# Performance work log

Measured on AMD Instinct MI355X. Metric: run time of the kernel, lower is better.

The kernel has to match this reference:

```python
import jax, jax.numpy as jnp
import numpy as np


def setup_inputs() -> dict:
    key = jax.random.key(0)
    k1, k2, k3, k4 = jax.random.split(key, 4)
    B, C, T = 32, 512, 1024
    N, D = 64, 512
    scale = 1.0 / np.sqrt(C)
    x = jax.random.normal(k1, (B, C, T), dtype=jnp.float32)
    subjects = jax.random.randint(k2, (B,), 0, N, dtype=jnp.int64)
    weights = jax.random.normal(k3, (N, C, D), dtype=jnp.float32) * scale
    bias = jax.random.normal(k4, (N, D), dtype=jnp.float32) * scale
    return {"x": x, "subjects": subjects, "weights": weights, "bias": bias}


def reference(x, subjects, weights, bias):
    # gather mode: per-example projection matrix, then batched GEMM
    # x: (B, C, T); weights[subjects]: (B, C, D) -> out: (B, D, T)
    w = weights[subjects]                      # (B, C, D)
    out = jnp.einsum('bct,bcd->bdt', x, w)
    out = out + bias[subjects][:, :, None]     # (B, D, 1) broadcast over T
    return out
```

## Files before the change

kernel.cpp:

```cpp
#include <hip/hip_runtime.h>
#include <hip/hip_bf16.h>

#define B_N 32
#define C_K 512
#define T_N 1024
#define D_M 512

constexpr int BM = 128, BN = 128, BK = 32;
constexpr int SA = 36;
constexpr int KSTEPS = C_K / BK;
constexpr int BUFO = BM * SA;

typedef __attribute__((ext_vector_type(4))) float  floatx4;
typedef __attribute__((ext_vector_type(4))) short  shortx4;
typedef __attribute__((ext_vector_type(8))) short  shortx8;
typedef __attribute__((ext_vector_type(2))) unsigned int uintx2;

__device__ __forceinline__ unsigned pk2(float a, float b) {
  __hip_bfloat162 h = __float22bfloat162_rn(make_float2(a, b));
  union { __hip_bfloat162 v; unsigned u; } c; c.v = h; return c.u;
}

__device__ __forceinline__ void wg_barrier() {
  asm volatile("s_waitcnt lgkmcnt(0)" ::: "memory");
  __builtin_amdgcn_s_barrier();
  __builtin_amdgcn_sched_barrier(0);
}

__global__ __launch_bounds__(512, 4)
void subject_gemm(const float* __restrict__ x, const int* __restrict__ subjects,
                  const float* __restrict__ weights, const float* __restrict__ bias,
                  float* __restrict__ out)
{
  __shared__ __align__(16) short lds_a[2][BUFO];
  __shared__ __align__(16) short lds_b[2][BUFO];

  const int bid  = blockIdx.x;
  const int xcd  = bid & 7;
  const int s    = bid >> 3;
  const int b    = xcd * 4 + (s & 3);
  const int tile = s >> 2;
  const int tm = tile >> 3, tn = tile & 7;
  const int m0 = tm * BM, n0 = tn * BN;
  const int nb = subjects[b];

  const float* __restrict__ Wp = weights + (size_t)nb * C_K * D_M;
  const float* __restrict__ Xp = x + (size_t)b * C_K * T_N;

  const int tid  = threadIdx.x;
  const int lane = tid & 63;
  const int wave = tid >> 6;

  const bool isA = (wave < 4);
  const int  wv  = wave & 3;
  const int  o   = lane >> 5;
  const int  mg  = lane & 31;
  const int  kq  = 2 * wv + o;
  const float* gsrc = isA ? (Wp + (size_t)(4 * kq) * D_M + (m0 + 4 * mg))
                          : (Xp + (size_t)(4 * kq) * T_N + (n0 + 4 * mg));
  const int gs = isA ? D_M : T_N;
  const int swz = (mg >> 2) & 3;
  short* const wbase = (isA ? &lds_a[0][0] : &lds_b[0][0])
                       + (4 * mg) * SA + 4 * (kq ^ swz);

  const int wm = (wave & 1) * 64, wn = (wave >> 1) * 32;
  const int w1 = (wave >> 1) & 1;
  const int l15 = lane & 15, q = lane >> 4;

  floatx4 acc[4][2] = {};
  floatx4 vA[4], vB[4];

  auto loads = [&](floatx4 (&v)[4]) {
    #pragma unroll
    for (int jj = 0; jj < 4; ++jj)
      v[jj] = *(const floatx4*)(gsrc + (size_t)jj * gs);
    gsrc += (size_t)BK * gs;
  };
  auto cvt_store = [&](const floatx4 (&v)[4], int p) {
    short* wdst = wbase + p * BUFO;
    #pragma unroll
    for (int r = 0; r < 4; ++r) {
      uintx2 pk = { pk2(v[0][r], v[1][r]), pk2(v[2][r], v[3][r]) };
      *(uintx2*)(wdst + r * SA) = pk;
    }
  };
  auto compute = [&](int p) {
    const short* pa = &lds_a[p][0] + (wm + l15) * SA;
    const short* pb = &lds_b[p][0] + (wn + l15) * SA;
    shortx8 af[4], bg[2];
    #pragma unroll
    for (int i = 0; i < 4; ++i) {
      const int base = 16 * i * SA + 8 * (q ^ (i >> 1));
      shortx4 alo = *(const shortx4*)(pa + base + 4 * (i & 1));
      shortx4 ahi = *(const shortx4*)(pa + base + 4 * ((i & 1) ^ 1));
      af[i] = __builtin_shufflevector(alo, ahi, 0, 1, 2, 3, 4, 5, 6, 7);
    }
    #pragma unroll
    for (int j = 0; j < 2; ++j) {
      const int base = 16 * j * SA + 8 * (q ^ w1);
      shortx4 blo = *(const shortx4*)(pb + base + 4 * j);
      shortx4 bhi = *(const shortx4*)(pb + base + 4 * (j ^ 1));
      bg[j] = __builtin_shufflevector(blo, bhi, 0, 1, 2, 3, 4, 5, 6, 7);
    }
    #pragma unroll
    for (int i = 0; i < 4; ++i)
      #pragma unroll
      for (int j = 0; j < 2; ++j)
        acc[i][j] = __builtin_amdgcn_mfma_f32_16x16x32_bf16(af[i], bg[j], acc[i][j], 0, 0, 0);
  };

  loads(vA);
  loads(vB);
  cvt_store(vA, 0);

  #pragma unroll 1
  for (int kk = 0; kk < KSTEPS - 2; kk += 2) {
    wg_barrier();
    loads(vA);
    compute(0);
    cvt_store(vB, 1);
    wg_barrier();
    loads(vB);
    compute(1);
    cvt_store(vA, 0);
  }
  wg_barrier();
  compute(0);
  cvt_store(vB, 1);
  wg_barrier();
  compute(1);

  float* __restrict__ O = out + (size_t)b * D_M * T_N;
  const float* __restrict__ bb = bias + (size_t)nb * D_M;
  #pragma unroll
  for (int i = 0; i < 4; ++i) {
    #pragma unroll
    for (int r = 0; r < 4; ++r) {
      const int d = m0 + wm + 16 * i + 4 * q + r;
      const float bv = bb[d];
      #pragma unroll
      for (int j = 0; j < 2; ++j) {
        const int t = n0 + wn + 16 * j + l15;
        O[(size_t)d * T_N + t] = acc[i][j][r] + bv;
      }
    }
  }
}

extern "C" void kernel_launch(void* const* d_in, const int* in_sizes, int n_in,
                              void* d_out, int out_size, void* d_ws, size_t ws_size,
                              hipStream_t stream) {
  const float* x        = (const float*)d_in[0];
  const int*   subjects = (const int*)d_in[1];
  const float* weights  = (const float*)d_in[2];
  const float* bias     = (const float*)d_in[3];
  float* out = (float*)d_out;
  (void)in_sizes; (void)n_in; (void)out_size; (void)d_ws; (void)ws_size;

  dim3 grid(B_N * 4 * 8);
  dim3 block(512);
  hipLaunchKernelGGL(subject_gemm, grid, block, 0, stream, x, subjects, weights, bias, out);
}
```

Baseline: 189.8 us.

## Use 256-thread blocks with 64x64 per-wave tiles and new LDS swizzle

Halves the workgroup to 4 waves, so each wave now computes a 64x64 output subtile (4x4 MFMA tiles) instead of 64x32. Each loader thread fetches 8 rows rather than 4. The LDS layout gets a new XOR swizzle for writes and fragment reads. The aim is better MFMA-to-LDS-read reuse per wave and less barrier cost per unit of work. The price is higher register pressure: 64 accumulator floats plus 16 staging float4s, with the launch bound cut to 3 blocks per CU.

Measured after the change: 184.3 us. 2.9% less time.

```diff
diff --git a/kernel.cpp b/kernel.cpp
--- a/kernel.cpp
+++ b/kernel.cpp
@@ -27,7 +27,7 @@
   __builtin_amdgcn_sched_barrier(0);
 }
 
-__global__ __launch_bounds__(512, 4)
+__global__ __launch_bounds__(256, 3)
 void subject_gemm(const float* __restrict__ x, const int* __restrict__ subjects,
                   const float* __restrict__ weights, const float* __restrict__ bias,
                   float* __restrict__ out)
@@ -51,61 +51,59 @@
   const int lane = tid & 63;
   const int wave = tid >> 6;
 
-  const bool isA = (wave < 4);
-  const int  wv  = wave & 3;
-  const int  o   = lane >> 5;
-  const int  mg  = lane & 31;
-  const int  kq  = 2 * wv + o;
-  const float* gsrc = isA ? (Wp + (size_t)(4 * kq) * D_M + (m0 + 4 * mg))
-                          : (Xp + (size_t)(4 * kq) * T_N + (n0 + 4 * mg));
+  const bool isA = (wave < 2);
+  const int  mg  = (wave & 1) * 16 + (lane & 15);
+  const int  oct = lane >> 4;
+  const float* gsrc = isA ? (Wp + (size_t)(8 * oct) * D_M + (m0 + 4 * mg))
+                          : (Xp + (size_t)(8 * oct) * T_N + (n0 + 4 * mg));
   const int gs = isA ? D_M : T_N;
-  const int swz = (mg >> 2) & 3;
-  short* const wbase = (isA ? &lds_a[0][0] : &lds_b[0][0])
-                       + (4 * mg) * SA + 4 * (kq ^ swz);
+  const int sw  = mg & 3;
+  const int cLo = 4 * ((2 * oct) ^ sw);
+  const int cHi = 4 * ((2 * oct + 1) ^ sw);
+  short* const wbase = (isA ? &lds_a[0][0] : &lds_b[0][0]) + (4 * mg) * SA;
 
-  const int wm = (wave & 1) * 64, wn = (wave >> 1) * 32;
-  const int w1 = (wave >> 1) & 1;
+  const int wm = (wave & 1) * 64, wn = (wave >> 1) * 64;
   const int l15 = lane & 15, q = lane >> 4;
+  const int sr  = (l15 >> 2) & 3;
+  const int rLo = 4 * ((2 * q) ^ sr);
+  const int rHi = 4 * ((2 * q + 1) ^ sr);
 
-  floatx4 acc[4][2] = {};
-  floatx4 vA[4], vB[4];
+  floatx4 acc[4][4] = {};
+  floatx4 vA[8], vB[8];
 
-  auto loads = [&](floatx4 (&v)[4]) {
+  auto loads = [&](floatx4 (&v)[8]) {
     #pragma unroll
-    for (int jj = 0; jj < 4; ++jj)
+    for (int jj = 0; jj < 8; ++jj)
       v[jj] = *(const floatx4*)(gsrc + (size_t)jj * gs);
     gsrc += (size_t)BK * gs;
   };
-  auto cvt_store = [&](const floatx4 (&v)[4], int p) {
+  auto cvt_store = [&](const floatx4 (&v)[8], int p) {
     short* wdst = wbase + p * BUFO;
     #pragma unroll
     for (int r = 0; r < 4; ++r) {
-      uintx2 pk = { pk2(v[0][r], v[1][r]), pk2(v[2][r], v[3][r]) };
-      *(uintx2*)(wdst + r * SA) = pk;
+      uintx2 lo = { pk2(v[0][r], v[1][r]), pk2(v[2][r], v[3][r]) };
+      uintx2 hi = { pk2(v[4][r], v[5][r]), pk2(v[6][r], v[7][r]) };
+      *(uintx2*)(wdst + r * SA + cLo) = lo;
+      *(uintx2*)(wdst + r * SA + cHi) = hi;
     }
   };
   auto compute = [&](int p) {
     const short* pa = &lds_a[p][0] + (wm + l15) * SA;
     const short* pb = &lds_b[p][0] + (wn + l15) * SA;
-    shortx8 af[4], bg[2];
+    shortx8 af[4], bg[4];
     #pragma unroll
     for (int i = 0; i < 4; ++i) {
-      const int base = 16 * i * SA + 8 * (q ^ (i >> 1));
-      shortx4 alo = *(const shortx4*)(pa + base + 4 * (i & 1));
-      shortx4 ahi = *(const shortx4*)(pa + base + 4 * ((i & 1) ^ 1));
+      shortx4 alo = *(const shortx4*)(pa + 16 * i * SA + rLo);
+      shortx4 ahi = *(const shortx4*)(pa + 16 * i * SA + rHi);
+      shortx4 blo = *(const shortx4*)(pb + 16 * i * SA + rLo);
+      shortx4 bhi = *(const shortx4*)(pb + 16 * i * SA + rHi);
       af[i] = __builtin_shufflevector(alo, ahi, 0, 1, 2, 3, 4, 5, 6, 7);
-    }
-    #pragma unroll
-    for (int j = 0; j < 2; ++j) {
-      const int base = 16 * j * SA + 8 * (q ^ w1);
-      shortx4 blo = *(const shortx4*)(pb + base + 4 * j);
-      shortx4 bhi = *(const shortx4*)(pb + base + 4 * (j ^ 1));
-      bg[j] = __builtin_shufflevector(blo, bhi, 0, 1, 2, 3, 4, 5, 6, 7);
+      bg[i] = __builtin_shufflevector(blo, bhi, 0, 1, 2, 3, 4, 5, 6, 7);
     }
     #pragma unroll
     for (int i = 0; i < 4; ++i)
       #pragma unroll
-      for (int j = 0; j < 2; ++j)
+      for (int j = 0; j < 4; ++j)
         acc[i][j] = __builtin_amdgcn_mfma_f32_16x16x32_bf16(af[i], bg[j], acc[i][j], 0, 0, 0);
   };
 
@@ -139,7 +137,7 @@
       const int d = m0 + wm + 16 * i + 4 * q + r;
       const float bv = bb[d];
       #pragma unroll
-      for (int j = 0; j < 2; ++j) {
+      for (int j = 0; j < 4; ++j) {
         const int t = n0 + wn + 16 * j + l15;
         O[(size_t)d * T_N + t] = acc[i][j][r] + bv;
       }
@@ -158,6 +156,6 @@
   (void)in_sizes; (void)n_in; (void)out_size; (void)d_ws; (void)ws_size;
 
   dim3 grid(B_N * 4 * 8);
-  dim3 block(512);
+  dim3 block(256);
   hipLaunchKernelGGL(subject_gemm, grid, block, 0, stream, x, subjects, weights, bias, out);
 }
```
